# Kernel optimization log

Hardware: AMD Instinct MI355X
Metric: run time of the kernel (lower is better)

## Reference

```python
import jax, jax.numpy as jnp
import numpy as np
from jax import lax


def setup_inputs() -> dict:
    key = jax.random.key(0)
    ks = jax.random.split(key, 4)
    B, Cin, H, W = 8, 64, 128, 128
    Cout, kh, kw = 64, 3, 3
    K = kh * kw
    x = jax.random.normal(ks[0], (B, Cin, H, W), jnp.float32)
    # small init so predicted offsets stay in a sensible range
    w_offset = jax.random.normal(ks[1], (2 * K, Cin, kh, kw), jnp.float32) * 0.01
    b_offset = jnp.zeros((2 * K,), jnp.float32)
    w_conv = jax.random.normal(ks[2], (Cout, Cin, kh, kw), jnp.float32) * (1.0 / np.sqrt(Cin * K))
    b_conv = jax.random.normal(ks[3], (Cout,), jnp.float32) * 0.01
    return dict(x=x, w_offset=w_offset, b_offset=b_offset, w_conv=w_conv, b_conv=b_conv)


def _deform_conv2d(x, offset, w, b, stride=(1, 1), padding=(1, 1), dilation=(1, 1)):
    B, Cin, Hin, Win = x.shape
    Cout, _, kh, kw = w.shape
    K = kh * kw
    sh, sw = stride; ph, pw = padding; dh, dw = dilation
    Hout = (Hin + 2 * ph - dh * (kh - 1) - 1) // sh + 1
    Wout = (Win + 2 * pw - dw * (kw - 1) - 1) // sw + 1
    # torchvision layout: [B, K, (dy,dx), Hout, Wout]
    off = offset.reshape(B, K, 2, Hout, Wout)
    dy, dx = off[:, :, 0], off[:, :, 1]
    hs = jnp.arange(Hout, dtype=x.dtype) * sh - ph          # [Hout]
    ws = jnp.arange(Wout, dtype=x.dtype) * sw - pw          # [Wout]
    ky = jnp.repeat(jnp.arange(kh, dtype=x.dtype) * dh, kw)  # [K]
    kx = jnp.tile(jnp.arange(kw, dtype=x.dtype) * dw, kh)    # [K]
    py = dy + (ky[:, None, None] + hs[None, :, None])[None]  # [B,K,Hout,Wout]
    px = dx + (kx[:, None, None] + ws[None, None, :])[None]

    def sample(img, py, px):
        y0 = jnp.floor(py); x0 = jnp.floor(px)
        wy1 = py - y0; wx1 = px - x0
        wy0 = 1.0 - wy1; wx0 = 1.0 - wx1

        def gather(yy, xx, wgt):
            valid = (yy >= 0) & (yy <= Hin - 1) & (xx >= 0) & (xx <= Win - 1)
            yi = jnp.clip(yy, 0, Hin - 1).astype(jnp.int32)
            xi = jnp.clip(xx, 0, Win - 1).astype(jnp.int32)
            vals = img[:, yi, xi]  # [Cin,K,Hout,Wout]
            return vals * (wgt * valid)[None]

        return (gather(y0, x0, wy0 * wx0) + gather(y0, x0 + 1, wy0 * wx1)
                + gather(y0 + 1, x0, wy1 * wx0) + gather(y0 + 1, x0 + 1, wy1 * wx1))

    sampled = jax.vmap(sample)(x, py, px)  # [B,Cin,K,Hout,Wout]
    out = jnp.einsum('bckhw,ock->bohw', sampled, w.reshape(Cout, Cin, K))
    return out + b[None, :, None, None]


def reference(x, w_offset, b_offset, w_conv, b_conv):
    # offset-predicting conv (stride 1, same padding, dilation 1)
    offset = lax.conv_general_dilated(
        x, w_offset, window_strides=(1, 1), padding=[(1, 1), (1, 1)],
        rhs_dilation=(1, 1), dimension_numbers=('NCHW', 'OIHW', 'NCHW'))
    offset = offset + b_offset[None, :, None, None]
    # deformable conv v1 (mask is None in _get_deformation)
    return _deform_conv2d(x, offset, w_conv, b_conv)
```

## Files before the change

kernel.cpp:

```cpp
#include <hip/hip_runtime.h>
#include <stdint.h>

#define H 128
#define W 128
#define CIN 64
#define COUT 64
#define NB 8
#define WR 4
#define WC 16
#define CW 20
#define PLANE 162
#define REDS 260

typedef __attribute__((ext_vector_type(4))) float f32x4;
typedef __attribute__((ext_vector_type(2))) _Float16 f16x2;
typedef __attribute__((ext_vector_type(8))) _Float16 f16x8;
typedef __attribute__((ext_vector_type(4))) unsigned int u32x4;
typedef __attribute__((ext_vector_type(2))) unsigned int u32x2;

__device__ __forceinline__ f16x2 bch2(unsigned u) { return __builtin_bit_cast(f16x2, u); }
__device__ __forceinline__ unsigned bcu(f16x2 v) { return __builtin_bit_cast(unsigned, v); }

__global__ __launch_bounds__(256) void x_to_nhwc(const float* __restrict__ x,
                                                 _Float16* __restrict__ xt) {
    __shared__ _Float16 tile[W][68];
    int bh = blockIdx.x;
    int h = bh & (H - 1), b = bh >> 7;
    int t = threadIdx.x;
    #pragma unroll
    for (int i = 0; i < 8; ++i) {
        int idx = i * 256 + t;
        int c = idx >> 5;
        int w4 = (idx & 31) << 2;
        f32x4 v = *(const f32x4*)(x + (((size_t)(b * CIN + c) * H + h) * W + w4));
        #pragma unroll
        for (int j = 0; j < 4; ++j) tile[w4 + j][c] = (_Float16)v[j];
    }
    __syncthreads();
    _Float16* dst = xt + (size_t)bh * W * CIN;
    #pragma unroll
    for (int i = 0; i < 8; ++i) {
        int idx = i * 256 + t;
        int w = idx >> 4;
        int c4 = (idx & 15) << 2;
        *(uint2*)(dst + (size_t)w * CIN + c4) = *(const uint2*)&tile[w][c4];
    }
}

__global__ __launch_bounds__(256) void prep_w(const float* __restrict__ wo,
                                              const float* __restrict__ wc,
                                              _Float16* __restrict__ wao2,
                                              _Float16* __restrict__ wac2) {
    int t = blockIdx.x * 256 + threadIdx.x;
    if (t < 18432) {
        int j = t & 7, l = (t >> 3) & 63, m = (t >> 9) & 1, kk = t >> 10;
        int cout = m * 16 + (l & 15);
        int cin = (kk & 1) * 32 + ((l >> 4) << 3) + j;
        wao2[t] = (cout < 18) ? (_Float16)wo[(cout * 64 + cin) * 9 + (kk >> 1)]
                              : (_Float16)0.f;
    } else if (t < 18432 + 36864) {
        int u = t - 18432;
        int j = u & 7, l = (u >> 3) & 63, m = (u >> 9) & 3, kk = u >> 11;
        int cout = m * 16 + (l & 15);
        int cin = (kk & 1) * 32 + ((l >> 4) << 3) + j;
        wac2[u] = (_Float16)wc[(cout * 64 + cin) * 9 + (kk >> 1)];
    }
}

__global__ __launch_bounds__(512, 5) void deform_fused(const _Float16* __restrict__ xt,
                                                       const _Float16* __restrict__ wao2,
                                                       const _Float16* __restrict__ wac2,
                                                       const float* __restrict__ bo,
                                                       const float* __restrict__ bconv,
                                                       float* __restrict__ out) {
    __shared__ u32x4 s_x[8 * PLANE];
    __shared__ float s_meta[4][432];

    int bid = blockIdx.x;
    int b = bid & 7;
    int r = bid >> 3;
    int h0 = ((r >> 3) & 31) << 2;
    int w0 = (r & 7) << 4;

    int r_lo = max(0, h0 - 2), r_hi = min(H - 1, h0 + 5);
    int c_lo = max(0, w0 - 2), c_hi = min(W - 1, w0 + WC + 1);
    int nr = r_hi - r_lo + 1, nc = c_hi - c_lo + 1;

    int t = threadIdx.x;
    int lane = t & 63, wv = t >> 6;
    int g = wv & 3;
    int half = wv >> 2;
    int pcol = lane & 15, hq = lane >> 4;
    int pl = half * 4 + hq;
    int h = h0 + g;
    int wp = w0 + pcol;

    const _Float16* xb = xt + (size_t)b * H * W * CIN;

    {
        int cs = t >> 3, ch = t & 7;
        bool act = t < nc * 8;
        for (int rr = 0; rr < nr; ++rr) {
            if (act) {
                u32x4 v = *(const u32x4*)(xb + (size_t)((r_lo + rr) * W + c_lo + cs) * CIN + (ch << 3));
                s_x[ch * PLANE + rr * CW + cs] = v;
            }
        }
    }
    __syncthreads();

    const u32x4* sp = s_x + pl * PLANE;

    f32x4 ao0 = {}, ao1 = {};
    #pragma unroll
    for (int k = 0; k < 9; ++k) {
        int yy = h + k / 3 - 1;
        int xx = wp + k % 3 - 1;
        bool valid = ((unsigned)yy < (unsigned)H) && ((unsigned)xx < (unsigned)W);
        int yc = min(max(yy, 0), H - 1);
        int xc = min(max(xx, 0), W - 1);
        int s = (yc - r_lo) * CW + (xc - c_lo);
        u32x4 v = sp[s];
        u32x4 z = {};
        if (!valid) v = z;
        f16x8 bf = __builtin_bit_cast(f16x8, v);
        const _Float16* wb = wao2 + (size_t)(4 * k + 2 * half) * 512 + lane * 8;
        ao0 = __builtin_amdgcn_mfma_f32_16x16x32_f16(*(const f16x8*)(wb), bf, ao0, 0, 0, 0);
        ao1 = __builtin_amdgcn_mfma_f32_16x16x32_f16(*(const f16x8*)(wb + 512), bf, ao1, 0, 0, 0);
    }

    if (half == 1) {
        float* sc = s_meta[g] + lane * 6;
        sc[0] = ao0[0]; sc[1] = ao0[1]; sc[2] = ao0[2]; sc[3] = ao0[3];
        sc[4] = ao1[0]; sc[5] = ao1[1];
    }
    __syncthreads();

    if (half == 0) {
        const float* sc = s_meta[g] + lane * 6;
        float p0 = sc[0], p1 = sc[1], p2 = sc[2], p3 = sc[3], p4 = sc[4], p5 = sc[5];
        ao0[0] += p0; ao0[1] += p1; ao0[2] += p2; ao0[3] += p3;
        ao1[0] += p4; ao1[1] += p5;

        auto setup = [&](int k, float dy, float dx) {
            float py = (float)(h + k / 3 - 1) + dy;
            float px = (float)(wp + k % 3 - 1) + dx;
            float y0f = floorf(py), x0f = floorf(px);
            float fy = py - y0f, fx = px - x0f;
            float vy0 = (y0f >= 0.f  && y0f <= 127.f) ? 1.f : 0.f;
            float vy1 = (y0f >= -1.f && y0f <= 126.f) ? 1.f : 0.f;
            float vx0 = (x0f >= 0.f  && x0f <= 127.f) ? 1.f : 0.f;
            float vx1 = (x0f >= -1.f && x0f <= 126.f) ? 1.f : 0.f;
            float g0 = (1.f - fy) * (1.f - fx) * vy0 * vx0;
            float g1 = (1.f - fy) * fx         * vy0 * vx1;
            float g2 = fy * (1.f - fx)         * vy1 * vx0;
            float g3 = fy * fx                 * vy1 * vx1;
            int y0i = (int)fminf(fmaxf(y0f, 0.f), 127.f);
            int x0i = (int)fminf(fmaxf(x0f, 0.f), 127.f);
            int y1i = (int)fminf(fmaxf(y0f + 1.f, 0.f), 127.f);
            int x1i = (int)fminf(fmaxf(x0f + 1.f, 0.f), 127.f);
            unsigned dxb = (unsigned)(x1i - x0i);
            unsigned dyb = (unsigned)(y1i - y0i);
            bool inw = (y0i >= r_lo) && (y1i <= r_hi) && (x0i >= c_lo) && (x1i <= c_hi);
            unsigned s00 = inw ? (unsigned)((y0i - r_lo) * CW + (x0i - c_lo)) : 0u;
            unsigned a00 = (unsigned)(y0i * W + x0i);
            unsigned awv = s00 | (dxb << 9) | (dyb << 10) | (inw ? 0u : (1u << 11)) | (a00 << 12);
            int idx = k * 16 + pcol;
            ((unsigned*)s_meta[g])[idx] = awv;
            ((unsigned*)s_meta[g])[144 + 2 * idx]     = bcu((f16x2){(_Float16)g0, (_Float16)g1});
            ((unsigned*)s_meta[g])[144 + 2 * idx + 1] = bcu((f16x2){(_Float16)g2, (_Float16)g3});
        };
        f32x4 bo4 = *(const f32x4*)(bo + 4 * hq);
        setup(2 * hq,     ao0[0] + bo4[0], ao0[1] + bo4[1]);
        setup(2 * hq + 1, ao0[2] + bo4[2], ao0[3] + bo4[3]);
        if (hq == 0) setup(8, ao1[0] + bo[16], ao1[1] + bo[17]);
    }
    __syncthreads();

    const _Float16* xh = xb + (pl << 3);
    f32x4 acc[4] = {};

    unsigned AW[9];
    #pragma unroll
    for (int k = 0; k < 9; ++k) AW[k] = ((unsigned*)s_meta[g])[k * 16 + pcol];

    u32x4 C0[4], C1[4];
    #define FETCH(kk, Cb)                                                      \
        {                                                                      \
            unsigned aw_ = AW[kk];                                             \
            unsigned s00_ = aw_ & 511u;                                        \
            unsigned dx_ = (aw_ >> 9) & 1u;                                    \
            unsigned dy_ = (aw_ >> 10) & 1u;                                   \
            unsigned s01_ = s00_ + dx_, s10_ = s00_ + dy_ * CW, s11_ = s10_ + dx_; \
            Cb[0] = sp[s00_]; Cb[1] = sp[s01_];                                \
            Cb[2] = sp[s10_]; Cb[3] = sp[s11_];                                \
        }

    FETCH(0, C0);
    #pragma unroll
    for (int k = 0; k < 9; ++k) {
        u32x4 c00, c01, c10, c11;
        if (k & 1) { c00 = C1[0]; c01 = C1[1]; c10 = C1[2]; c11 = C1[3]; }
        else       { c00 = C0[0]; c01 = C0[1]; c10 = C0[2]; c11 = C0[3]; }
        if (k < 8) {
            if (k & 1) { FETCH(k + 1, C0) }
            else       { FETCH(k + 1, C1) }
        }
        unsigned aw = AW[k];
        u32x2 wq = *(const u32x2*)&((unsigned*)s_meta[g])[144 + 2 * (k * 16 + pcol)];
        if (__builtin_expect((aw & (1u << 11)) != 0u, 0)) {
            unsigned dxb = (aw >> 9) & 1u;
            unsigned dyb = (aw >> 10) & 1u;
            unsigned a00 = aw >> 12;
            unsigned a01 = a00 + dxb;
            unsigned a10 = a00 + (dyb << 7);
            unsigned a11 = a10 + dxb;
            c00 = *(const u32x4*)(xh + (size_t)a00 * CIN);
            c01 = *(const u32x4*)(xh + (size_t)a01 * CIN);
            c10 = *(const u32x4*)(xh + (size_t)a10 * CIN);
            c11 = *(const u32x4*)(xh + (size_t)a11 * CIN);
        }
        f16x2 wab = bch2(wq[0]);
        f16x2 wcd = bch2(wq[1]);
        f16x2 w00d = (f16x2){wab[0], wab[0]};
        f16x2 w01d = (f16x2){wab[1], wab[1]};
        f16x2 w10d = (f16x2){wcd[0], wcd[0]};
        f16x2 w11d = (f16x2){wcd[1], wcd[1]};
        u32x4 fr;
        #pragma unroll
        for (int d = 0; d < 4; ++d) {
            f16x2 v = bch2(c00[d]) * w00d + bch2(c01[d]) * w01d
                    + bch2(c10[d]) * w10d + bch2(c11[d]) * w11d;
            fr[d] = bcu(v);
        }
        f16x8 bf = __builtin_bit_cast(f16x8, fr);
        const _Float16* ab = wac2 + (size_t)(8 * k + 4 * half) * 512 + lane * 8;
        #pragma unroll
        for (int m = 0; m < 4; ++m)
            acc[m] = __builtin_amdgcn_mfma_f32_16x16x32_f16(*(const f16x8*)(ab + m * 512), bf, acc[m], 0, 0, 0);
    }
    #undef FETCH

    __syncthreads();
    float* red = (float*)s_x;
    if (half == 0) {
        #pragma unroll
        for (int m = 0; m < 4; ++m)
            #pragma unroll
            for (int r2 = 0; r2 < 4; ++r2)
                red[(m * 4 + r2) * REDS + g * 64 + lane] = acc[m][r2];
    }
    __syncthreads();
    if (half == 1) {
        #pragma unroll
        for (int m = 0; m < 4; ++m) {
            f32x4 bc4 = *(const f32x4*)(bconv + m * 16 + (hq << 2));
            #pragma unroll
            for (int r2 = 0; r2 < 4; ++r2) {
                int co = (m << 4) + (hq << 2) + r2;
                float v = acc[m][r2] + red[(m * 4 + r2) * REDS + g * 64 + lane] + bc4[r2];
                out[(((size_t)b * COUT + co) * H + h) * W + wp] = v;
            }
        }
    }
}

extern "C" void kernel_launch(void* const* d_in, const int* in_sizes, int n_in,
                              void* d_out, int out_size, void* d_ws, size_t ws_size,
                              hipStream_t stream) {
    const float* x  = (const float*)d_in[0];
    const float* wo = (const float*)d_in[1];
    const float* bo = (const float*)d_in[2];
    const float* wc = (const float*)d_in[3];
    const float* bc = (const float*)d_in[4];
    float* out = (float*)d_out;

    _Float16* xt   = (_Float16*)d_ws;
    _Float16* wao2 = (_Float16*)((char*)d_ws + (size_t)NB * H * W * CIN * 2);
    _Float16* wac2 = wao2 + 18432;

    x_to_nhwc<<<NB * H, 256, 0, stream>>>(x, xt);
    prep_w<<<(18432 + 36864 + 255) / 256, 256, 0, stream>>>(wo, wc, wao2, wac2);
    deform_fused<<<NB * H * W / (WR * WC), 512, 0, stream>>>(xt, wao2, wac2, bo, bc, out);
}
```

Baseline: 54.74 us.

## Precompute byte offsets and broadcast weights in metadata, drop register prefetch

```diff
diff --git a/kernel.cpp b/kernel.cpp
--- a/kernel.cpp
+++ b/kernel.cpp
@@ -67,14 +67,15 @@
     }
 }
 
-__global__ __launch_bounds__(512, 5) void deform_fused(const _Float16* __restrict__ xt,
+__global__ __launch_bounds__(512, 4) void deform_fused(const _Float16* __restrict__ xt,
                                                        const _Float16* __restrict__ wao2,
                                                        const _Float16* __restrict__ wac2,
                                                        const float* __restrict__ bo,
                                                        const float* __restrict__ bconv,
                                                        float* __restrict__ out) {
     __shared__ u32x4 s_x[8 * PLANE];
-    __shared__ float s_meta[4][432];
+    __shared__ u32x4 s_m0[4][144];
+    __shared__ u32x4 s_m1[4][144];
 
     int bid = blockIdx.x;
     int b = bid & 7;
@@ -130,14 +131,14 @@
     }
 
     if (half == 1) {
-        float* sc = s_meta[g] + lane * 6;
+        float* sc = (float*)&s_m0[g][0] + lane * 6;
         sc[0] = ao0[0]; sc[1] = ao0[1]; sc[2] = ao0[2]; sc[3] = ao0[3];
         sc[4] = ao1[0]; sc[5] = ao1[1];
     }
     __syncthreads();
 
     if (half == 0) {
-        const float* sc = s_meta[g] + lane * 6;
+        const float* sc = (const float*)&s_m0[g][0] + lane * 6;
         float p0 = sc[0], p1 = sc[1], p2 = sc[2], p3 = sc[3], p4 = sc[4], p5 = sc[5];
         ao0[0] += p0; ao0[1] += p1; ao0[2] += p2; ao0[3] += p3;
         ao1[0] += p4; ao1[1] += p5;
@@ -159,16 +160,29 @@
             int x0i = (int)fminf(fmaxf(x0f, 0.f), 127.f);
             int y1i = (int)fminf(fmaxf(y0f + 1.f, 0.f), 127.f);
             int x1i = (int)fminf(fmaxf(x0f + 1.f, 0.f), 127.f);
-            unsigned dxb = (unsigned)(x1i - x0i);
-            unsigned dyb = (unsigned)(y1i - y0i);
             bool inw = (y0i >= r_lo) && (y1i <= r_hi) && (x0i >= c_lo) && (x1i <= c_hi);
-            unsigned s00 = inw ? (unsigned)((y0i - r_lo) * CW + (x0i - c_lo)) : 0u;
-            unsigned a00 = (unsigned)(y0i * W + x0i);
-            unsigned awv = s00 | (dxb << 9) | (dyb << 10) | (inw ? 0u : (1u << 11)) | (a00 << 12);
-            int idx = k * 16 + pcol;
-            ((unsigned*)s_meta[g])[idx] = awv;
-            ((unsigned*)s_meta[g])[144 + 2 * idx]     = bcu((f16x2){(_Float16)g0, (_Float16)g1});
-            ((unsigned*)s_meta[g])[144 + 2 * idx + 1] = bcu((f16x2){(_Float16)g2, (_Float16)g3});
+            u32x4 m0;
+            if (inw) {
+                unsigned s00 = (unsigned)((y0i - r_lo) * CW + (x0i - c_lo));
+                unsigned dxb = (unsigned)(x1i - x0i);
+                unsigned dyb = (unsigned)(y1i - y0i);
+                m0[0] = s00 * 16u;
+                m0[1] = (s00 + dxb) * 16u;
+                m0[2] = (s00 + dyb * CW) * 16u;
+                m0[3] = (s00 + dyb * CW + dxb) * 16u;
+            } else {
+                m0[0] = ((unsigned)(y0i * W + x0i) * 128u) | 1u;
+                m0[1] = (unsigned)(y0i * W + x1i) * 128u;
+                m0[2] = (unsigned)(y1i * W + x0i) * 128u;
+                m0[3] = (unsigned)(y1i * W + x1i) * 128u;
+            }
+            u32x4 m1;
+            m1[0] = bcu((f16x2){(_Float16)g0, (_Float16)g0});
+            m1[1] = bcu((f16x2){(_Float16)g1, (_Float16)g1});
+            m1[2] = bcu((f16x2){(_Float16)g2, (_Float16)g2});
+            m1[3] = bcu((f16x2){(_Float16)g3, (_Float16)g3});
+            s_m0[g][k * 16 + pcol] = m0;
+            s_m1[g][k * 16 + pcol] = m1;
         };
         f32x4 bo4 = *(const f32x4*)(bo + 4 * hq);
         setup(2 * hq,     ao0[0] + bo4[0], ao0[1] + bo4[1]);
@@ -177,55 +191,26 @@
     }
     __syncthreads();
 
-    const _Float16* xh = xb + (pl << 3);
+    const char* lb = (const char*)s_x + pl * (PLANE * 16);
+    const char* gb = (const char*)xb + (pl << 4);
     f32x4 acc[4] = {};
 
-    unsigned AW[9];
-    #pragma unroll
-    for (int k = 0; k < 9; ++k) AW[k] = ((unsigned*)s_meta[g])[k * 16 + pcol];
-
-    u32x4 C0[4], C1[4];
-    #define FETCH(kk, Cb)                                                      \
-        {                                                                      \
-            unsigned aw_ = AW[kk];                                             \
-            unsigned s00_ = aw_ & 511u;                                        \
-            unsigned dx_ = (aw_ >> 9) & 1u;                                    \
-            unsigned dy_ = (aw_ >> 10) & 1u;                                   \
-            unsigned s01_ = s00_ + dx_, s10_ = s00_ + dy_ * CW, s11_ = s10_ + dx_; \
-            Cb[0] = sp[s00_]; Cb[1] = sp[s01_];                                \
-            Cb[2] = sp[s10_]; Cb[3] = sp[s11_];                                \
-        }
-
-    FETCH(0, C0);
     #pragma unroll
     for (int k = 0; k < 9; ++k) {
-        u32x4 c00, c01, c10, c11;
-        if (k & 1) { c00 = C1[0]; c01 = C1[1]; c10 = C1[2]; c11 = C1[3]; }
-        else       { c00 = C0[0]; c01 = C0[1]; c10 = C0[2]; c11 = C0[3]; }
-        if (k < 8) {
-            if (k & 1) { FETCH(k + 1, C0) }
-            else       { FETCH(k + 1, C1) }
-        }
-        unsigned aw = AW[k];
-        u32x2 wq = *(const u32x2*)&((unsigned*)s_meta[g])[144 + 2 * (k * 16 + pcol)];
-        if (__builtin_expect((aw & (1u << 11)) != 0u, 0)) {
-            unsigned dxb = (aw >> 9) & 1u;
-            unsigned dyb = (aw >> 10) & 1u;
-            unsigned a00 = aw >> 12;
-            unsigned a01 = a00 + dxb;
-            unsigned a10 = a00 + (dyb << 7);
-            unsigned a11 = a10 + dxb;
-            c00 = *(const u32x4*)(xh + (size_t)a00 * CIN);
-            c01 = *(const u32x4*)(xh + (size_t)a01 * CIN);
-            c10 = *(const u32x4*)(xh + (size_t)a10 * CIN);
-            c11 = *(const u32x4*)(xh + (size_t)a11 * CIN);
-        }
-        f16x2 wab = bch2(wq[0]);
-        f16x2 wcd = bch2(wq[1]);
-        f16x2 w00d = (f16x2){wab[0], wab[0]};
-        f16x2 w01d = (f16x2){wab[1], wab[1]};
-        f16x2 w10d = (f16x2){wcd[0], wcd[0]};
-        f16x2 w11d = (f16x2){wcd[1], wcd[1]};
+        u32x4 m0 = s_m0[g][k * 16 + pcol];
+        u32x4 m1 = s_m1[g][k * 16 + pcol];
+        u32x4 c00 = *(const u32x4*)(lb + (m0[0] & 0xFFFFFFFEu));
+        u32x4 c01 = *(const u32x4*)(lb + m0[1]);
+        u32x4 c10 = *(const u32x4*)(lb + m0[2]);
+        u32x4 c11 = *(const u32x4*)(lb + m0[3]);
+        if (__builtin_expect((m0[0] & 1u) != 0u, 0)) {
+            c00 = *(const u32x4*)(gb + (m0[0] & 0xFFFFFFFEu));
+            c01 = *(const u32x4*)(gb + m0[1]);
+            c10 = *(const u32x4*)(gb + m0[2]);
+            c11 = *(const u32x4*)(gb + m0[3]);
+        }
+        f16x2 w00d = bch2(m1[0]), w01d = bch2(m1[1]);
+        f16x2 w10d = bch2(m1[2]), w11d = bch2(m1[3]);
         u32x4 fr;
         #pragma unroll
         for (int d = 0; d < 4; ++d) {
@@ -235,11 +220,12 @@
         }
         f16x8 bf = __builtin_bit_cast(f16x8, fr);
         const _Float16* ab = wac2 + (size_t)(8 * k + 4 * half) * 512 + lane * 8;
+        __builtin_amdgcn_s_setprio(1);
         #pragma unroll
         for (int m = 0; m < 4; ++m)
             acc[m] = __builtin_amdgcn_mfma_f32_16x16x32_f16(*(const f16x8*)(ab + m * 512), bf, acc[m], 0, 0, 0);
-    }
-    #undef FETCH
+        __builtin_amdgcn_s_setprio(0);
+    }
 
     __syncthreads();
     float* red = (float*)s_x;
```

Result: slower. 66.33 us (+21.2%).

## Deepen software pipeline to prefetch LDS samples and MFMA weights two taps ahead

Applied to the files above, without the earlier changes.

```diff
diff --git a/kernel.cpp b/kernel.cpp
--- a/kernel.cpp
+++ b/kernel.cpp
@@ -67,7 +67,7 @@
     }
 }
 
-__global__ __launch_bounds__(512, 5) void deform_fused(const _Float16* __restrict__ xt,
+__global__ __launch_bounds__(512, 4) void deform_fused(const _Float16* __restrict__ xt,
                                                        const _Float16* __restrict__ wao2,
                                                        const _Float16* __restrict__ wac2,
                                                        const float* __restrict__ bo,
@@ -181,65 +181,90 @@
     f32x4 acc[4] = {};
 
     unsigned AW[9];
-    #pragma unroll
-    for (int k = 0; k < 9; ++k) AW[k] = ((unsigned*)s_meta[g])[k * 16 + pcol];
-
-    u32x4 C0[4], C1[4];
-    #define FETCH(kk, Cb)                                                      \
-        {                                                                      \
-            unsigned aw_ = AW[kk];                                             \
-            unsigned s00_ = aw_ & 511u;                                        \
-            unsigned dx_ = (aw_ >> 9) & 1u;                                    \
-            unsigned dy_ = (aw_ >> 10) & 1u;                                   \
-            unsigned s01_ = s00_ + dx_, s10_ = s00_ + dy_ * CW, s11_ = s10_ + dx_; \
-            Cb[0] = sp[s00_]; Cb[1] = sp[s01_];                                \
-            Cb[2] = sp[s10_]; Cb[3] = sp[s11_];                                \
-        }
-
-    FETCH(0, C0);
+    u32x2   WQv[9];
     #pragma unroll
     for (int k = 0; k < 9; ++k) {
-        u32x4 c00, c01, c10, c11;
-        if (k & 1) { c00 = C1[0]; c01 = C1[1]; c10 = C1[2]; c11 = C1[3]; }
-        else       { c00 = C0[0]; c01 = C0[1]; c10 = C0[2]; c11 = C0[3]; }
-        if (k < 8) {
-            if (k & 1) { FETCH(k + 1, C0) }
-            else       { FETCH(k + 1, C1) }
-        }
-        unsigned aw = AW[k];
-        u32x2 wq = *(const u32x2*)&((unsigned*)s_meta[g])[144 + 2 * (k * 16 + pcol)];
-        if (__builtin_expect((aw & (1u << 11)) != 0u, 0)) {
-            unsigned dxb = (aw >> 9) & 1u;
-            unsigned dyb = (aw >> 10) & 1u;
-            unsigned a00 = aw >> 12;
-            unsigned a01 = a00 + dxb;
-            unsigned a10 = a00 + (dyb << 7);
-            unsigned a11 = a10 + dxb;
-            c00 = *(const u32x4*)(xh + (size_t)a00 * CIN);
-            c01 = *(const u32x4*)(xh + (size_t)a01 * CIN);
-            c10 = *(const u32x4*)(xh + (size_t)a10 * CIN);
-            c11 = *(const u32x4*)(xh + (size_t)a11 * CIN);
-        }
-        f16x2 wab = bch2(wq[0]);
-        f16x2 wcd = bch2(wq[1]);
-        f16x2 w00d = (f16x2){wab[0], wab[0]};
-        f16x2 w01d = (f16x2){wab[1], wab[1]};
-        f16x2 w10d = (f16x2){wcd[0], wcd[0]};
-        f16x2 w11d = (f16x2){wcd[1], wcd[1]};
-        u32x4 fr;
-        #pragma unroll
-        for (int d = 0; d < 4; ++d) {
-            f16x2 v = bch2(c00[d]) * w00d + bch2(c01[d]) * w01d
-                    + bch2(c10[d]) * w10d + bch2(c11[d]) * w11d;
-            fr[d] = bcu(v);
-        }
-        f16x8 bf = __builtin_bit_cast(f16x8, fr);
-        const _Float16* ab = wac2 + (size_t)(8 * k + 4 * half) * 512 + lane * 8;
-        #pragma unroll
-        for (int m = 0; m < 4; ++m)
-            acc[m] = __builtin_amdgcn_mfma_f32_16x16x32_f16(*(const f16x8*)(ab + m * 512), bf, acc[m], 0, 0, 0);
-    }
-    #undef FETCH
+        AW[k]  = ((unsigned*)s_meta[g])[k * 16 + pcol];
+        WQv[k] = *(const u32x2*)&((unsigned*)s_meta[g])[144 + 2 * (k * 16 + pcol)];
+    }
+
+    u32x4 cA0, cA1, cA2, cA3, cB0, cB1, cB2, cB3;
+    f16x8 wA0, wA1, wA2, wA3, wB0, wB1, wB2, wB3;
+
+#define ISSUE(kk, C0, C1, C2, C3, V0, V1, V2, V3) {                           \
+        unsigned aw_ = AW[kk];                                                \
+        unsigned s00_ = aw_ & 511u;                                           \
+        unsigned dx_ = (aw_ >> 9) & 1u;                                       \
+        unsigned dy_ = (aw_ >> 10) & 1u;                                      \
+        C0 = sp[s00_];            C1 = sp[s00_ + dx_];                        \
+        C2 = sp[s00_ + dy_ * CW]; C3 = sp[s00_ + dy_ * CW + dx_];             \
+        const _Float16* ab_ = wac2 + (size_t)(8 * (kk) + 4 * half) * 512 + lane * 8; \
+        V0 = *(const f16x8*)(ab_);        V1 = *(const f16x8*)(ab_ + 512);    \
+        V2 = *(const f16x8*)(ab_ + 1024); V3 = *(const f16x8*)(ab_ + 1536);   \
+    }
+
+#define BODY(kk, C0, C1, C2, C3, V0, V1, V2, V3) {                            \
+        unsigned aw_ = AW[kk];                                                \
+        if (__builtin_expect((aw_ & (1u << 11)) != 0u, 0)) {                  \
+            unsigned dxb_ = (aw_ >> 9) & 1u;                                  \
+            unsigned dyb_ = (aw_ >> 10) & 1u;                                 \
+            unsigned a00_ = aw_ >> 12;                                        \
+            c00 = *(const u32x4*)(xh + (size_t)a00_ * CIN);                   \
+            c01 = *(const u32x4*)(xh + (size_t)(a00_ + dxb_) * CIN);          \
+            c10 = *(const u32x4*)(xh + (size_t)(a00_ + (dyb_ << 7)) * CIN);   \
+            c11 = *(const u32x4*)(xh + (size_t)(a00_ + (dyb_ << 7) + dxb_) * CIN); \
+        }                                                                     \
+        u32x2 wq_ = WQv[kk];                                                  \
+        f16x2 wab_ = bch2(wq_[0]);                                            \
+        f16x2 wcd_ = bch2(wq_[1]);                                            \
+        f16x2 w00d = (f16x2){wab_[0], wab_[0]};                               \
+        f16x2 w01d = (f16x2){wab_[1], wab_[1]};                               \
+        f16x2 w10d = (f16x2){wcd_[0], wcd_[0]};                               \
+        f16x2 w11d = (f16x2){wcd_[1], wcd_[1]};                               \
+        u32x4 fr_;                                                            \
+        _Pragma("unroll")                                                     \
+        for (int d = 0; d < 4; ++d) {                                         \
+            f16x2 v_ = bch2(c00[d]) * w00d + bch2(c01[d]) * w01d              \
+                     + bch2(c10[d]) * w10d + bch2(c11[d]) * w11d;             \
+            fr_[d] = bcu(v_);                                                 \
+        }                                                                     \
+        f16x8 bf_ = __builtin_bit_cast(f16x8, fr_);                           \
+        acc[0] = __builtin_amdgcn_mfma_f32_16x16x32_f16(V0, bf_, acc[0], 0, 0, 0); \
+        acc[1] = __builtin_amdgcn_mfma_f32_16x16x32_f16(V1, bf_, acc[1], 0, 0, 0); \
+        acc[2] = __builtin_amdgcn_mfma_f32_16x16x32_f16(V2, bf_, acc[2], 0, 0, 0); \
+        acc[3] = __builtin_amdgcn_mfma_f32_16x16x32_f16(V3, bf_, acc[3], 0, 0, 0); \
+    }
+
+#define STEPI(kk, C0, C1, C2, C3, V0, V1, V2, V3) {                           \
+        u32x4 c00 = C0, c01 = C1, c10 = C2, c11 = C3;                         \
+        f16x8 v0_ = V0, v1_ = V1, v2_ = V2, v3_ = V3;                         \
+        ISSUE(kk + 2, C0, C1, C2, C3, V0, V1, V2, V3);                        \
+        __builtin_amdgcn_sched_barrier(0);                                    \
+        BODY(kk, c00, c01, c10, c11, v0_, v1_, v2_, v3_);                     \
+    }
+#define STEPN(kk, C0, C1, C2, C3, V0, V1, V2, V3) {                           \
+        u32x4 c00 = C0, c01 = C1, c10 = C2, c11 = C3;                         \
+        f16x8 v0_ = V0, v1_ = V1, v2_ = V2, v3_ = V3;                         \
+        __builtin_amdgcn_sched_barrier(0);                                    \
+        BODY(kk, c00, c01, c10, c11, v0_, v1_, v2_, v3_);                     \
+    }
+
+    ISSUE(0, cA0, cA1, cA2, cA3, wA0, wA1, wA2, wA3);
+    ISSUE(1, cB0, cB1, cB2, cB3, wB0, wB1, wB2, wB3);
+    __builtin_amdgcn_sched_barrier(0);
+    STEPI(0, cA0, cA1, cA2, cA3, wA0, wA1, wA2, wA3);
+    STEPI(1, cB0, cB1, cB2, cB3, wB0, wB1, wB2, wB3);
+    STEPI(2, cA0, cA1, cA2, cA3, wA0, wA1, wA2, wA3);
+    STEPI(3, cB0, cB1, cB2, cB3, wB0, wB1, wB2, wB3);
+    STEPI(4, cA0, cA1, cA2, cA3, wA0, wA1, wA2, wA3);
+    STEPI(5, cB0, cB1, cB2, cB3, wB0, wB1, wB2, wB3);
+    STEPI(6, cA0, cA1, cA2, cA3, wA0, wA1, wA2, wA3);
+    STEPN(7, cB0, cB1, cB2, cB3, wB0, wB1, wB2, wB3);
+    STEPN(8, cA0, cA1, cA2, cA3, wA0, wA1, wA2, wA3);
+#undef ISSUE
+#undef BODY
+#undef STEPI
+#undef STEPN
 
     __syncthreads();
     float* red = (float*)s_x;
```

Measured after the change: 109.9 us. +100.8%, slower.
